# Kernel optimization log

Hardware: AMD Instinct MI355X
Metric: run time of the kernel (lower is better)

Reference implementation:

```python
import jax, jax.numpy as jnp
import numpy as np
import math

B, H, L, D = 4, 16, 8192, 64


def setup_inputs() -> dict:
    key = jax.random.key(0)
    kq, kk, kv, kmu = jax.random.split(key, 4)
    Q = jax.random.normal(kq, (B, H, L, D), dtype=jnp.float32)
    K = jax.random.normal(kk, (B, H, L, D), dtype=jnp.float32)
    V = jax.random.normal(kv, (B, H, L, D), dtype=jnp.float32)
    mask = jnp.ones((B, L), dtype=jnp.float32)
    # learned params (multi_gauss=True): pi init [0.5,0.5]; mu ~ N(0,0.5) with mu[0]=0
    pi = jnp.array([0.5, 0.5], dtype=jnp.float32)
    mu = jax.random.normal(kmu, (2, H, D), dtype=jnp.float32) * 0.5
    mu = mu * jnp.array([0.0, 1.0], dtype=jnp.float32)[:, None, None]
    return {"Q": Q, "K": K, "V": V, "mask": mask, "pi": pi, "mu": mu}


def reference(Q, K, V, mask, pi, mu):
    # mixture-of-Gaussian keys: shift K by two learned means, convex-combine
    p = jnp.clip(pi, 0.0, 1.0)
    K1 = K - mu[0][None, :, None, :]
    K2 = K - mu[1][None, :, None, :]
    Km = K1 * p[0] + K2 * p[1]
    # kernelized linear attention: phi(x) = elu(x)+1, scaled by 1/L^0.25
    L_ = Q.shape[2]
    s = 1.0 / math.sqrt(math.sqrt(L_))
    m = mask[:, None, :, None]  # [B,1,L,1]
    Qf = (jax.nn.elu(Q) + 1.0) * s
    Kf = (jax.nn.elu(Km) + 1.0) * m * s
    Vm = V * m
    # K^T V first: [B,H,D,D] state, then Q @ state -> [B,H,L,D]
    KV = jnp.einsum('bhld,bhle->bhde', Kf, Vm)
    return jnp.einsum('bhld,bhde->bhle', Qf, KV)
```

## Files before the change

kernel.cpp:

```cpp
#include <hip/hip_runtime.h>
#include <cstddef>
#include <stdint.h>

#define B_ 4
#define H_ 16
#define L_ 8192
#define D_ 64
#define BH_ 64

#define SCALE 0.1051120519067143f

__device__ __forceinline__ float elu1(float x) {
    return x > 0.0f ? (x + 1.0f) : __expf(x);
}
__device__ __forceinline__ unsigned short f2bf_rne(float x) {
    unsigned u = __float_as_uint(x);
    u += 0x7fffu + ((u >> 16) & 1u);
    return (unsigned short)(u >> 16);
}
__device__ __forceinline__ float bf_lo(unsigned w) { return __uint_as_float(w << 16); }
__device__ __forceinline__ float bf_hi(unsigned w) { return __uint_as_float(w & 0xffff0000u); }

__global__ __launch_bounds__(256) void zero_kernel(float4* __restrict__ p) {
    p[(size_t)blockIdx.x * 256 + threadIdx.x] = make_float4(0.f, 0.f, 0.f, 0.f);
}

#define CH1 16
#define ROWS1 (L_ / CH1)
#define TR1 64
#define SKLD 68

__global__ __launch_bounds__(256, 4) void kv_kernel(
    const float* __restrict__ K, const float* __restrict__ V,
    const float* __restrict__ mask, const float* __restrict__ pi,
    const float* __restrict__ mu, float* __restrict__ kv)
{
    __shared__ float sK[TR1 * SKLD];
    __shared__ float muc[64];

    const int bh = blockIdx.x;
    const int b  = bh >> 4;
    const int h  = bh & 15;
    const int l0 = blockIdx.y * ROWS1;
    const int t  = threadIdx.x;
    const int wave = t >> 6;
    const int lane = t & 63;
    const int d0 = (lane >> 3) * 8;
    const int e0 = (lane & 7) * 8;

    const float p0 = fminf(fmaxf(pi[0], 0.f), 1.f);
    const float p1 = fminf(fmaxf(pi[1], 0.f), 1.f);
    const float psum = p0 + p1;
    if (t < 64) muc[t] = p0 * mu[h * 64 + t] + p1 * mu[1024 + h * 64 + t];

    const float* Kb = K + (size_t)bh * (L_ * 64);
    const float* Vb = V + (size_t)bh * (L_ * 64);
    const float* mb = mask + (size_t)b * L_;

    const int trow = t >> 2;
    const int tc   = (t & 3) * 16;

    float acc[64];
#pragma unroll
    for (int i = 0; i < 64; ++i) acc[i] = 0.f;

#pragma unroll 1
    for (int tile = 0; tile < ROWS1; tile += TR1) {
        const int base = l0 + tile;
        __syncthreads();
        {
            const int row = base + trow;
            const float m = mb[row];
            const float sm2 = SCALE * m * m;
            const float* kp = Kb + (size_t)row * 64 + tc;
#pragma unroll
            for (int q = 0; q < 4; ++q) {
                float4 kk = *(const float4*)(kp + 4 * q);
                float4 mm = *(const float4*)(&muc[tc + 4 * q]);
                float4 o;
                o.x = elu1(kk.x * psum - mm.x) * sm2;
                o.y = elu1(kk.y * psum - mm.y) * sm2;
                o.z = elu1(kk.z * psum - mm.z) * sm2;
                o.w = elu1(kk.w * psum - mm.w) * sm2;
                *(float4*)&sK[trow * SKLD + tc + 4 * q] = o;
            }
        }
        __syncthreads();
#pragma unroll
        for (int j = 0; j < 16; ++j) {
            const int r = wave + 4 * j;
            const float* vp = Vb + (size_t)(base + r) * 64 + e0;
            const float4 va = *(const float4*)(vp);
            const float4 vb = *(const float4*)(vp + 4);
            const float4 ka = *(const float4*)&sK[r * SKLD + d0];
            const float4 kb = *(const float4*)&sK[r * SKLD + d0 + 4];
            const float kf[8] = {ka.x, ka.y, ka.z, ka.w, kb.x, kb.y, kb.z, kb.w};
            const float vf[8] = {va.x, va.y, va.z, va.w, vb.x, vb.y, vb.z, vb.w};
#pragma unroll
            for (int i = 0; i < 8; ++i)
#pragma unroll
                for (int jj = 0; jj < 8; ++jj)
                    acc[i * 8 + jj] = fmaf(kf[i], vf[jj], acc[i * 8 + jj]);
        }
    }

    __syncthreads();
    float* red = sK;
#pragma unroll 1
    for (int w = 0; w < 4; ++w) {
        if (wave == w) {
#pragma unroll
            for (int i = 0; i < 8; ++i)
#pragma unroll
                for (int jj = 0; jj < 8; ++jj) {
                    const int idx = (d0 + i) * 64 + e0 + jj;
                    red[idx] = (w == 0) ? acc[i * 8 + jj] : red[idx] + acc[i * 8 + jj];
                }
        }
        __syncthreads();
    }

    float* kvb = kv + (size_t)bh * 4096;
#pragma unroll
    for (int k = 0; k < 16; ++k)
        atomicAdd(kvb + k * 256 + t, red[k * 256 + t]);
}

#define ROWS2 256

__global__ __launch_bounds__(256, 3) void out_kernel(
    const float* __restrict__ Q, const float* __restrict__ kv,
    float* __restrict__ out)
{
    __shared__ unsigned short skv[64 * 64];
    __shared__ unsigned short sqt[4][64 * 64];

    const int bh = blockIdx.x;
    const int l0 = blockIdx.y * ROWS2;
    const int t = threadIdx.x;
    const int wave = t >> 6;
    const int lane = t & 63;
    const int r0 = (lane >> 3) * 8;
    const int e0 = (lane & 7) * 8;

    {
        const float* kvb = kv + (size_t)bh * 4096 + t * 16;
        unsigned w[8];
#pragma unroll
        for (int q = 0; q < 4; ++q) {
            float4 f = *(const float4*)(kvb + 4 * q);
            w[2 * q + 0] = (unsigned)f2bf_rne(f.x) | ((unsigned)f2bf_rne(f.y) << 16);
            w[2 * q + 1] = (unsigned)f2bf_rne(f.z) | ((unsigned)f2bf_rne(f.w) << 16);
        }
        *(uint4*)&skv[t * 16 + 0] = make_uint4(w[0], w[1], w[2], w[3]);
        *(uint4*)&skv[t * 16 + 8] = make_uint4(w[4], w[5], w[6], w[7]);
    }
    {
        const int row = l0 + wave * 64 + lane;
        const float* qp = Q + (size_t)bh * (L_ * 64) + (size_t)row * 64;
        unsigned short* qt = &sqt[wave][0];
#pragma unroll
        for (int c4 = 0; c4 < 16; ++c4) {
            float4 q = *(const float4*)(qp + 4 * c4);
            qt[(4 * c4 + 0) * 64 + lane] = f2bf_rne(elu1(q.x) * SCALE);
            qt[(4 * c4 + 1) * 64 + lane] = f2bf_rne(elu1(q.y) * SCALE);
            qt[(4 * c4 + 2) * 64 + lane] = f2bf_rne(elu1(q.z) * SCALE);
            qt[(4 * c4 + 3) * 64 + lane] = f2bf_rne(elu1(q.w) * SCALE);
        }
    }
    __syncthreads();

    float acc[64];
#pragma unroll
    for (int i = 0; i < 64; ++i) acc[i] = 0.f;

    const unsigned short* qt = &sqt[wave][0];
#pragma unroll 1
    for (int c = 0; c < 16; ++c) {
#pragma unroll
        for (int k = 0; k < 4; ++k) {
            const int d = 4 * c + k;
            const uint4 qw = *(const uint4*)&qt[d * 64 + r0];
            const uint4 kw = *(const uint4*)&skv[d * 64 + e0];
            const float qf[8] = {bf_lo(qw.x), bf_hi(qw.x), bf_lo(qw.y), bf_hi(qw.y),
                                 bf_lo(qw.z), bf_hi(qw.z), bf_lo(qw.w), bf_hi(qw.w)};
            const float kf[8] = {bf_lo(kw.x), bf_hi(kw.x), bf_lo(kw.y), bf_hi(kw.y),
                                 bf_lo(kw.z), bf_hi(kw.z), bf_lo(kw.w), bf_hi(kw.w)};
#pragma unroll
            for (int i = 0; i < 8; ++i)
#pragma unroll
                for (int j = 0; j < 8; ++j)
                    acc[i * 8 + j] = fmaf(qf[i], kf[j], acc[i * 8 + j]);
        }
    }

    float* ob = out + (size_t)bh * (L_ * 64) + (size_t)(l0 + wave * 64 + r0) * 64 + e0;
#pragma unroll
    for (int i = 0; i < 8; ++i) {
        float4 oa, obv;
        oa.x = acc[i * 8 + 0]; oa.y = acc[i * 8 + 1];
        oa.z = acc[i * 8 + 2]; oa.w = acc[i * 8 + 3];
        obv.x = acc[i * 8 + 4]; obv.y = acc[i * 8 + 5];
        obv.z = acc[i * 8 + 6]; obv.w = acc[i * 8 + 7];
        *(float4*)(ob + (size_t)i * 64) = oa;
        *(float4*)(ob + (size_t)i * 64 + 4) = obv;
    }
}

extern "C" void kernel_launch(void* const* d_in, const int* in_sizes, int n_in,
                              void* d_out, int out_size, void* d_ws, size_t ws_size,
                              hipStream_t stream) {
    (void)in_sizes; (void)n_in; (void)out_size; (void)ws_size;
    const float* Q    = (const float*)d_in[0];
    const float* K    = (const float*)d_in[1];
    const float* V    = (const float*)d_in[2];
    const float* mask = (const float*)d_in[3];
    const float* pi   = (const float*)d_in[4];
    const float* mu   = (const float*)d_in[5];
    float* out = (float*)d_out;
    float* kvw = (float*)d_ws;

    zero_kernel<<<256, 256, 0, stream>>>((float4*)kvw);
    kv_kernel<<<dim3(BH_, CH1), 256, 0, stream>>>(K, V, mask, pi, mu, kvw);
    out_kernel<<<dim3(BH_, L_ / ROWS2), 256, 0, stream>>>(Q, kvw, out);
}
```

Before: 518.8 us.

## Move both linear-attention GEMMs to bf16 MFMA with transposed LDS tiles

Both kernels replace scalar FMA outer-product accumulation with 16x16x32 bf16 MFMA instructions. K features and V are converted to bf16 and staged transposed in LDS, and the KV grid doubles its row splits, which means twice as many atomic adds. The output kernel keeps KV fragments in registers and streams Q directly from global memory with software prefetch of the next tile, with no LDS staging of Q. The aim is to cut the VALU compute cost and leave the kernels memory-bound, at the cost of bf16 rounding of V and K in the KV product and more atomic traffic.

```diff
diff --git a/kernel.cpp b/kernel.cpp
--- a/kernel.cpp
+++ b/kernel.cpp
@@ -2,51 +2,45 @@
 #include <cstddef>
 #include <stdint.h>
 
-#define B_ 4
-#define H_ 16
 #define L_ 8192
-#define D_ 64
 #define BH_ 64
-
 #define SCALE 0.1051120519067143f
+#define SLD 72
+
+typedef __attribute__((ext_vector_type(8))) short bf16x8;
+typedef __attribute__((ext_vector_type(4))) float f32x4;
 
 __device__ __forceinline__ float elu1(float x) {
     return x > 0.0f ? (x + 1.0f) : __expf(x);
 }
-__device__ __forceinline__ unsigned short f2bf_rne(float x) {
+__device__ __forceinline__ unsigned short f2bf(float x) {
     unsigned u = __float_as_uint(x);
     u += 0x7fffu + ((u >> 16) & 1u);
     return (unsigned short)(u >> 16);
 }
-__device__ __forceinline__ float bf_lo(unsigned w) { return __uint_as_float(w << 16); }
-__device__ __forceinline__ float bf_hi(unsigned w) { return __uint_as_float(w & 0xffff0000u); }
 
 __global__ __launch_bounds__(256) void zero_kernel(float4* __restrict__ p) {
     p[(size_t)blockIdx.x * 256 + threadIdx.x] = make_float4(0.f, 0.f, 0.f, 0.f);
 }
 
-#define CH1 16
-#define ROWS1 (L_ / CH1)
-#define TR1 64
-#define SKLD 68
-
-__global__ __launch_bounds__(256, 4) void kv_kernel(
+__global__ __launch_bounds__(256) void kv_kernel(
     const float* __restrict__ K, const float* __restrict__ V,
     const float* __restrict__ mask, const float* __restrict__ pi,
     const float* __restrict__ mu, float* __restrict__ kv)
 {
-    __shared__ float sK[TR1 * SKLD];
+    __shared__ __align__(16) unsigned short sKt[64 * SLD];
+    __shared__ __align__(16) unsigned short sVt[64 * SLD];
     __shared__ float muc[64];
 
     const int bh = blockIdx.x;
     const int b  = bh >> 4;
     const int h  = bh & 15;
-    const int l0 = blockIdx.y * ROWS1;
-    const int t  = threadIdx.x;
+    const int l0 = blockIdx.y * 256;
+    const int t    = threadIdx.x;
     const int wave = t >> 6;
     const int lane = t & 63;
-    const int d0 = (lane >> 3) * 8;
-    const int e0 = (lane & 7) * 8;
+    const int r = lane & 15;
+    const int q = lane >> 4;
 
     const float p0 = fminf(fmaxf(pi[0], 0.f), 1.f);
     const float p1 = fminf(fmaxf(pi[1], 0.f), 1.f);
@@ -57,153 +51,140 @@
     const float* Vb = V + (size_t)bh * (L_ * 64);
     const float* mb = mask + (size_t)b * L_;
 
-    const int trow = t >> 2;
-    const int tc   = (t & 3) * 16;
-
-    float acc[64];
-#pragma unroll
-    for (int i = 0; i < 64; ++i) acc[i] = 0.f;
+    const int lloc = t >> 2;
+    const int cb   = t & 3;
+
+    f32x4 acc[4];
+#pragma unroll
+    for (int i = 0; i < 4; ++i) acc[i] = (f32x4){0.f, 0.f, 0.f, 0.f};
+
+    __syncthreads();
 
 #pragma unroll 1
-    for (int tile = 0; tile < ROWS1; tile += TR1) {
-        const int base = l0 + tile;
+    for (int tile = 0; tile < 4; ++tile) {
+        const int lrow = l0 + tile * 64 + lloc;
+        const float m = mb[lrow];
+        const float sm2 = SCALE * m * m;
+        const float* kp = Kb + (size_t)lrow * 64;
+        const float* vp = Vb + (size_t)lrow * 64;
+        if (tile) __syncthreads();
+#pragma unroll
+        for (int i = 0; i < 4; ++i) {
+            const int c4 = cb + 4 * i;
+            const float4 kk = *(const float4*)(kp + 4 * c4);
+            const float4 mm = *(const float4*)(&muc[4 * c4]);
+            sKt[(4 * c4 + 0) * SLD + lloc] = f2bf(elu1(kk.x * psum - mm.x) * sm2);
+            sKt[(4 * c4 + 1) * SLD + lloc] = f2bf(elu1(kk.y * psum - mm.y) * sm2);
+            sKt[(4 * c4 + 2) * SLD + lloc] = f2bf(elu1(kk.z * psum - mm.z) * sm2);
+            sKt[(4 * c4 + 3) * SLD + lloc] = f2bf(elu1(kk.w * psum - mm.w) * sm2);
+            const float4 vv = *(const float4*)(vp + 4 * c4);
+            sVt[(4 * c4 + 0) * SLD + lloc] = f2bf(vv.x);
+            sVt[(4 * c4 + 1) * SLD + lloc] = f2bf(vv.y);
+            sVt[(4 * c4 + 2) * SLD + lloc] = f2bf(vv.z);
+            sVt[(4 * c4 + 3) * SLD + lloc] = f2bf(vv.w);
+        }
         __syncthreads();
-        {
-            const int row = base + trow;
-            const float m = mb[row];
-            const float sm2 = SCALE * m * m;
-            const float* kp = Kb + (size_t)row * 64 + tc;
-#pragma unroll
-            for (int q = 0; q < 4; ++q) {
-                float4 kk = *(const float4*)(kp + 4 * q);
-                float4 mm = *(const float4*)(&muc[tc + 4 * q]);
-                float4 o;
-                o.x = elu1(kk.x * psum - mm.x) * sm2;
-                o.y = elu1(kk.y * psum - mm.y) * sm2;
-                o.z = elu1(kk.z * psum - mm.z) * sm2;
-                o.w = elu1(kk.w * psum - mm.w) * sm2;
-                *(float4*)&sK[trow * SKLD + tc + 4 * q] = o;
-            }
-        }
-        __syncthreads();
-#pragma unroll
-        for (int j = 0; j < 16; ++j) {
-            const int r = wave + 4 * j;
-            const float* vp = Vb + (size_t)(base + r) * 64 + e0;
-            const float4 va = *(const float4*)(vp);
-            const float4 vb = *(const float4*)(vp + 4);
-            const float4 ka = *(const float4*)&sK[r * SKLD + d0];
-            const float4 kb = *(const float4*)&sK[r * SKLD + d0 + 4];
-            const float kf[8] = {ka.x, ka.y, ka.z, ka.w, kb.x, kb.y, kb.z, kb.w};
-            const float vf[8] = {va.x, va.y, va.z, va.w, vb.x, vb.y, vb.z, vb.w};
-#pragma unroll
-            for (int i = 0; i < 8; ++i)
-#pragma unroll
-                for (int jj = 0; jj < 8; ++jj)
-                    acc[i * 8 + jj] = fmaf(kf[i], vf[jj], acc[i * 8 + jj]);
-        }
-    }
-
-    __syncthreads();
-    float* red = sK;
-#pragma unroll 1
-    for (int w = 0; w < 4; ++w) {
-        if (wave == w) {
-#pragma unroll
-            for (int i = 0; i < 8; ++i)
-#pragma unroll
-                for (int jj = 0; jj < 8; ++jj) {
-                    const int idx = (d0 + i) * 64 + e0 + jj;
-                    red[idx] = (w == 0) ? acc[i * 8 + jj] : red[idx] + acc[i * 8 + jj];
-                }
-        }
-        __syncthreads();
+
+        const bf16x8 a0 = *(const bf16x8*)&sKt[(16 * wave + r) * SLD + 8 * q];
+        const bf16x8 a1 = *(const bf16x8*)&sKt[(16 * wave + r) * SLD + 32 + 8 * q];
+#pragma unroll
+        for (int nt = 0; nt < 4; ++nt) {
+            const bf16x8 b0 = *(const bf16x8*)&sVt[(16 * nt + r) * SLD + 8 * q];
+            const bf16x8 b1 = *(const bf16x8*)&sVt[(16 * nt + r) * SLD + 32 + 8 * q];
+            acc[nt] = __builtin_amdgcn_mfma_f32_16x16x32_bf16(a0, b0, acc[nt], 0, 0, 0);
+            acc[nt] = __builtin_amdgcn_mfma_f32_16x16x32_bf16(a1, b1, acc[nt], 0, 0, 0);
+        }
     }
 
     float* kvb = kv + (size_t)bh * 4096;
 #pragma unroll
-    for (int k = 0; k < 16; ++k)
-        atomicAdd(kvb + k * 256 + t, red[k * 256 + t]);
-}
-
-#define ROWS2 256
-
-__global__ __launch_bounds__(256, 3) void out_kernel(
+    for (int nt = 0; nt < 4; ++nt)
+#pragma unroll
+        for (int reg = 0; reg < 4; ++reg)
+            atomicAdd(kvb + (16 * wave + 4 * q + reg) * 64 + 16 * nt + r, acc[nt][reg]);
+}
+
+__global__ __launch_bounds__(256) void out_kernel(
     const float* __restrict__ Q, const float* __restrict__ kv,
     float* __restrict__ out)
 {
-    __shared__ unsigned short skv[64 * 64];
-    __shared__ unsigned short sqt[4][64 * 64];
+    __shared__ __align__(16) unsigned short sKVt[64 * SLD];
 
     const int bh = blockIdx.x;
-    const int l0 = blockIdx.y * ROWS2;
-    const int t = threadIdx.x;
+    const int l0 = blockIdx.y * 512;
+    const int t    = threadIdx.x;
     const int wave = t >> 6;
     const int lane = t & 63;
-    const int r0 = (lane >> 3) * 8;
-    const int e0 = (lane & 7) * 8;
+    const int r = lane & 15;
+    const int q = lane >> 4;
 
     {
         const float* kvb = kv + (size_t)bh * 4096 + t * 16;
-        unsigned w[8];
-#pragma unroll
-        for (int q = 0; q < 4; ++q) {
-            float4 f = *(const float4*)(kvb + 4 * q);
-            w[2 * q + 0] = (unsigned)f2bf_rne(f.x) | ((unsigned)f2bf_rne(f.y) << 16);
-            w[2 * q + 1] = (unsigned)f2bf_rne(f.z) | ((unsigned)f2bf_rne(f.w) << 16);
-        }
-        *(uint4*)&skv[t * 16 + 0] = make_uint4(w[0], w[1], w[2], w[3]);
-        *(uint4*)&skv[t * 16 + 8] = make_uint4(w[4], w[5], w[6], w[7]);
-    }
-    {
-        const int row = l0 + wave * 64 + lane;
-        const float* qp = Q + (size_t)bh * (L_ * 64) + (size_t)row * 64;
-        unsigned short* qt = &sqt[wave][0];
-#pragma unroll
-        for (int c4 = 0; c4 < 16; ++c4) {
-            float4 q = *(const float4*)(qp + 4 * c4);
-            qt[(4 * c4 + 0) * 64 + lane] = f2bf_rne(elu1(q.x) * SCALE);
-            qt[(4 * c4 + 1) * 64 + lane] = f2bf_rne(elu1(q.y) * SCALE);
-            qt[(4 * c4 + 2) * 64 + lane] = f2bf_rne(elu1(q.z) * SCALE);
-            qt[(4 * c4 + 3) * 64 + lane] = f2bf_rne(elu1(q.w) * SCALE);
+        const int d  = t >> 2;
+        const int e0 = (t & 3) * 16;
+#pragma unroll
+        for (int j4 = 0; j4 < 4; ++j4) {
+            const float4 f = *(const float4*)(kvb + 4 * j4);
+            sKVt[(e0 + 4 * j4 + 0) * SLD + d] = f2bf(f.x);
+            sKVt[(e0 + 4 * j4 + 1) * SLD + d] = f2bf(f.y);
+            sKVt[(e0 + 4 * j4 + 2) * SLD + d] = f2bf(f.z);
+            sKVt[(e0 + 4 * j4 + 3) * SLD + d] = f2bf(f.w);
         }
     }
     __syncthreads();
 
-    float acc[64];
-#pragma unroll
-    for (int i = 0; i < 64; ++i) acc[i] = 0.f;
-
-    const unsigned short* qt = &sqt[wave][0];
+    bf16x8 bfr[4][2];
+#pragma unroll
+    for (int nt = 0; nt < 4; ++nt) {
+        bfr[nt][0] = *(const bf16x8*)&sKVt[(16 * nt + r) * SLD + 8 * q];
+        bfr[nt][1] = *(const bf16x8*)&sKVt[(16 * nt + r) * SLD + 32 + 8 * q];
+    }
+
+    const int mbase = l0 + wave * 128;
+    const float* qrow = Q + (size_t)bh * (L_ * 64) + (size_t)(mbase + r) * 64 + 8 * q;
+    float* ob = out + (size_t)bh * (L_ * 64);
+
+    float4 c0 = *(const float4*)(qrow);
+    float4 c1 = *(const float4*)(qrow + 4);
+    float4 c2 = *(const float4*)(qrow + 32);
+    float4 c3 = *(const float4*)(qrow + 36);
+
 #pragma unroll 1
-    for (int c = 0; c < 16; ++c) {
-#pragma unroll
-        for (int k = 0; k < 4; ++k) {
-            const int d = 4 * c + k;
-            const uint4 qw = *(const uint4*)&qt[d * 64 + r0];
-            const uint4 kw = *(const uint4*)&skv[d * 64 + e0];
-            const float qf[8] = {bf_lo(qw.x), bf_hi(qw.x), bf_lo(qw.y), bf_hi(qw.y),
-                                 bf_lo(qw.z), bf_hi(qw.z), bf_lo(qw.w), bf_hi(qw.w)};
-            const float kf[8] = {bf_lo(kw.x), bf_hi(kw.x), bf_lo(kw.y), bf_hi(kw.y),
-                                 bf_lo(kw.z), bf_hi(kw.z), bf_lo(kw.w), bf_hi(kw.w)};
-#pragma unroll
-            for (int i = 0; i < 8; ++i)
-#pragma unroll
-                for (int j = 0; j < 8; ++j)
-                    acc[i * 8 + j] = fmaf(qf[i], kf[j], acc[i * 8 + j]);
-        }
-    }
-
-    float* ob = out + (size_t)bh * (L_ * 64) + (size_t)(l0 + wave * 64 + r0) * 64 + e0;
-#pragma unroll
-    for (int i = 0; i < 8; ++i) {
-        float4 oa, obv;
-        oa.x = acc[i * 8 + 0]; oa.y = acc[i * 8 + 1];
-        oa.z = acc[i * 8 + 2]; oa.w = acc[i * 8 + 3];
-        obv.x = acc[i * 8 + 4]; obv.y = acc[i * 8 + 5];
-        obv.z = acc[i * 8 + 6]; obv.w = acc[i * 8 + 7];
-        *(float4*)(ob + (size_t)i * 64) = oa;
-        *(float4*)(ob + (size_t)i * 64 + 4) = obv;
+    for (int mt = 0; mt < 8; ++mt) {
+        float4 n0, n1, n2, n3;
+        if (mt < 7) {
+            const float* nq = qrow + (size_t)(mt + 1) * 16 * 64;
+            n0 = *(const float4*)(nq);
+            n1 = *(const float4*)(nq + 4);
+            n2 = *(const float4*)(nq + 32);
+            n3 = *(const float4*)(nq + 36);
+        }
+        bf16x8 a0, a1;
+        a0[0] = f2bf(elu1(c0.x) * SCALE); a0[1] = f2bf(elu1(c0.y) * SCALE);
+        a0[2] = f2bf(elu1(c0.z) * SCALE); a0[3] = f2bf(elu1(c0.w) * SCALE);
+        a0[4] = f2bf(elu1(c1.x) * SCALE); a0[5] = f2bf(elu1(c1.y) * SCALE);
+        a0[6] = f2bf(elu1(c1.z) * SCALE); a0[7] = f2bf(elu1(c1.w) * SCALE);
+        a1[0] = f2bf(elu1(c2.x) * SCALE); a1[1] = f2bf(elu1(c2.y) * SCALE);
+        a1[2] = f2bf(elu1(c2.z) * SCALE); a1[3] = f2bf(elu1(c2.w) * SCALE);
+        a1[4] = f2bf(elu1(c3.x) * SCALE); a1[5] = f2bf(elu1(c3.y) * SCALE);
+        a1[6] = f2bf(elu1(c3.z) * SCALE); a1[7] = f2bf(elu1(c3.w) * SCALE);
+
+        f32x4 acc[4];
+#pragma unroll
+        for (int nt = 0; nt < 4; ++nt) {
+            acc[nt] = (f32x4){0.f, 0.f, 0.f, 0.f};
+            acc[nt] = __builtin_amdgcn_mfma_f32_16x16x32_bf16(a0, bfr[nt][0], acc[nt], 0, 0, 0);
+            acc[nt] = __builtin_amdgcn_mfma_f32_16x16x32_bf16(a1, bfr[nt][1], acc[nt], 0, 0, 0);
+        }
+
+        float* orow = ob + (size_t)(mbase + mt * 16 + 4 * q) * 64;
+#pragma unroll
+        for (int nt = 0; nt < 4; ++nt)
+#pragma unroll
+            for (int reg = 0; reg < 4; ++reg)
+                orow[(size_t)reg * 64 + 16 * nt + r] = acc[nt][reg];
+
+        c0 = n0; c1 = n1; c2 = n2; c3 = n3;
     }
 }
 
@@ -221,6 +202,6 @@
     float* kvw = (float*)d_ws;
 
     zero_kernel<<<256, 256, 0, stream>>>((float4*)kvw);
-    kv_kernel<<<dim3(BH_, CH1), 256, 0, stream>>>(K, V, mask, pi, mu, kvw);
-    out_kernel<<<dim3(BH_, L_ / ROWS2), 256, 0, stream>>>(Q, kvw, out);
-}
+    kv_kernel<<<dim3(BH_, 32), 256, 0, stream>>>(K, V, mask, pi, mu, kvw);
+    out_kernel<<<dim3(BH_, 16), 256, 0, stream>>>(Q, kvw, out);
+}
```

After: 419.1 us. -19.2%, faster.
